# Performance work log

Measured on AMD Instinct MI355X. Metric: run time of the kernel, lower is better.

Reference implementation:

```python
import jax, jax.numpy as jnp
import numpy as np

B, N = 4096, 2048


def _nrmse(o, t):
    # o, t: [B, 1, N]. Per-sample RMSE over all non-batch elements,
    # normalized by per-sample (max - min) of the target.
    rmse = jnp.sqrt(jnp.mean((o - t) ** 2, axis=(1, 2)))        # [B]
    rng = jnp.max(t, axis=(1, 2)) - jnp.min(t, axis=(1, 2))     # [B]
    return rmse / rng


def setup_inputs() -> dict:
    key = jax.random.key(0)
    ks = jax.random.split(key, 6)
    names = ["o1", "t1", "o2", "t2", "o3", "t3"]
    return {n: jax.random.normal(k, (B, 1, N), dtype=jnp.float32) for n, k in zip(names, ks)}


def reference(o1, t1, o2, t2, o3, t3):
    loss = (0.5 * _nrmse(o1, t1)
            + 0.25 * _nrmse(o2, t2)
            + 0.25 * _nrmse(o3, t3))  # [B]
    return jnp.mean(loss)
```

## Files before the change

### kernel.cpp

```cpp
#include <hip/hip_runtime.h>
#include <math.h>

constexpr int N_ELEM = 2048;
constexpr int BATCH  = 4096;
constexpr int BLOCK  = 256;
constexpr int GRID1  = 1536;
constexpr int WAVES1 = GRID1 * (BLOCK / 64);
constexpr int TASKS  = 3 * BATCH;

__global__ __launch_bounds__(BLOCK)
void wnrmse_stage1(const float* __restrict__ o1, const float* __restrict__ t1,
                   const float* __restrict__ o2, const float* __restrict__ t2,
                   const float* __restrict__ o3, const float* __restrict__ t3,
                   float* __restrict__ partial)
{
    const int tid  = threadIdx.x;
    const int wave = tid >> 6;
    const int lane = tid & 63;
    const int gw   = blockIdx.x * (BLOCK / 64) + wave;

    const float* const os[3] = { o1, o2, o3 };
    const float* const ts[3] = { t1, t2, t3 };
    const float wgt[3] = { 0.50f, 0.25f, 0.25f };

    float local = 0.0f;

    for (int task = gw; task < TASKS; task += WAVES1) {
        const int pair = task >> 12;
        const int row  = task & (BATCH - 1);

        const float4* o4 = (const float4*)(os[pair] + (size_t)row * N_ELEM);
        const float4* t4 = (const float4*)(ts[pair] + (size_t)row * N_ELEM);

        float ssd  = 0.0f;
        float tmax = -INFINITY;
        float tmin =  INFINITY;

#pragma unroll
        for (int j = 0; j < (N_ELEM / 4) / 64; ++j) {
            const int i = lane + j * 64;
            float4 ov = o4[i];
            float4 tv = t4[i];
            float d0 = ov.x - tv.x;
            float d1 = ov.y - tv.y;
            float d2 = ov.z - tv.z;
            float d3 = ov.w - tv.w;
            ssd += d0 * d0 + d1 * d1 + d2 * d2 + d3 * d3;
            tmax = fmaxf(tmax, fmaxf(fmaxf(tv.x, tv.y), fmaxf(tv.z, tv.w)));
            tmin = fminf(tmin, fminf(fminf(tv.x, tv.y), fminf(tv.z, tv.w)));
        }

#pragma unroll
        for (int off = 32; off > 0; off >>= 1) {
            ssd  += __shfl_xor(ssd, off, 64);
            tmax  = fmaxf(tmax, __shfl_xor(tmax, off, 64));
            tmin  = fminf(tmin, __shfl_xor(tmin, off, 64));
        }

        float rmse = sqrtf(ssd * (1.0f / (float)N_ELEM));
        local += wgt[pair] * rmse / (tmax - tmin);
    }

    __shared__ float s_part[BLOCK / 64];
    if (lane == 0) s_part[wave] = local;
    __syncthreads();
    if (tid == 0) {
        partial[blockIdx.x] = s_part[0] + s_part[1] + s_part[2] + s_part[3];
    }
}

__global__ __launch_bounds__(BLOCK)
void wnrmse_stage2(const float* __restrict__ partial, float* __restrict__ out)
{
    const int tid = threadIdx.x;
    float s = 0.0f;
    for (int i = tid; i < GRID1; i += BLOCK) s += partial[i];

#pragma unroll
    for (int off = 32; off > 0; off >>= 1) s += __shfl_xor(s, off, 64);

    __shared__ float s_part[BLOCK / 64];
    const int wave = tid >> 6;
    const int lane = tid & 63;
    if (lane == 0) s_part[wave] = s;
    __syncthreads();
    if (tid == 0) {
        float tot = s_part[0] + s_part[1] + s_part[2] + s_part[3];
        out[0] = tot * (1.0f / (float)BATCH);
    }
}

extern "C" void kernel_launch(void* const* d_in, const int* in_sizes, int n_in,
                              void* d_out, int out_size, void* d_ws, size_t ws_size,
                              hipStream_t stream) {
    const float* o1 = (const float*)d_in[0];
    const float* t1 = (const float*)d_in[1];
    const float* o2 = (const float*)d_in[2];
    const float* t2 = (const float*)d_in[3];
    const float* o3 = (const float*)d_in[4];
    const float* t3 = (const float*)d_in[5];
    float* out     = (float*)d_out;
    float* partial = (float*)d_ws;

    wnrmse_stage1<<<GRID1, BLOCK, 0, stream>>>(o1, t1, o2, t2, o3, t3, partial);
    wnrmse_stage2<<<1, BLOCK, 0, stream>>>(partial, out);
}
```

Before: 203.3 us.

## Launch one wave per row and batch all row loads before reducing

Replaces the grid-stride loop over rows with one wave per row, growing the grid to 3072 blocks. All 16 float4 loads for a row are issued up front into registers, and the squared-difference sum is split across four accumulators. The aim is more memory-level parallelism and shorter dependency chains in a bandwidth-bound reduction. In exchange it raises register use and the stage-2 partial count, and adds block launch and scheduling overhead.

```diff
diff --git a/kernel.cpp b/kernel.cpp
--- a/kernel.cpp
+++ b/kernel.cpp
@@ -4,9 +4,8 @@
 constexpr int N_ELEM = 2048;
 constexpr int BATCH  = 4096;
 constexpr int BLOCK  = 256;
-constexpr int GRID1  = 1536;
-constexpr int WAVES1 = GRID1 * (BLOCK / 64);
 constexpr int TASKS  = 3 * BATCH;
+constexpr int GRID1  = TASKS / (BLOCK / 64);
 
 __global__ __launch_bounds__(BLOCK)
 void wnrmse_stage1(const float* __restrict__ o1, const float* __restrict__ t1,
@@ -17,52 +16,56 @@
     const int tid  = threadIdx.x;
     const int wave = tid >> 6;
     const int lane = tid & 63;
-    const int gw   = blockIdx.x * (BLOCK / 64) + wave;
+    const int task = blockIdx.x * (BLOCK / 64) + wave;
 
-    const float* const os[3] = { o1, o2, o3 };
-    const float* const ts[3] = { t1, t2, t3 };
-    const float wgt[3] = { 0.50f, 0.25f, 0.25f };
+    const int pair = task >> 12;
+    const int row  = task & (BATCH - 1);
 
-    float local = 0.0f;
+    const float* o;
+    const float* t;
+    float w;
+    if (pair == 0)      { o = o1; t = t1; w = 0.50f; }
+    else if (pair == 1) { o = o2; t = t2; w = 0.25f; }
+    else                { o = o3; t = t3; w = 0.25f; }
 
-    for (int task = gw; task < TASKS; task += WAVES1) {
-        const int pair = task >> 12;
-        const int row  = task & (BATCH - 1);
+    const float4* o4 = (const float4*)(o + (size_t)row * N_ELEM);
+    const float4* t4 = (const float4*)(t + (size_t)row * N_ELEM);
 
-        const float4* o4 = (const float4*)(os[pair] + (size_t)row * N_ELEM);
-        const float4* t4 = (const float4*)(ts[pair] + (size_t)row * N_ELEM);
+    float4 ov[8], tv[8];
+#pragma unroll
+    for (int j = 0; j < 8; ++j) ov[j] = o4[lane + j * 64];
+#pragma unroll
+    for (int j = 0; j < 8; ++j) tv[j] = t4[lane + j * 64];
 
-        float ssd  = 0.0f;
-        float tmax = -INFINITY;
-        float tmin =  INFINITY;
+    float s0 = 0.f, s1 = 0.f, s2 = 0.f, s3 = 0.f;
+    float tmax = -INFINITY, tmin = INFINITY;
+#pragma unroll
+    for (int j = 0; j < 8; ++j) {
+        float d0 = ov[j].x - tv[j].x;
+        float d1 = ov[j].y - tv[j].y;
+        float d2 = ov[j].z - tv[j].z;
+        float d3 = ov[j].w - tv[j].w;
+        s0 += d0 * d0;
+        s1 += d1 * d1;
+        s2 += d2 * d2;
+        s3 += d3 * d3;
+        tmax = fmaxf(tmax, fmaxf(fmaxf(tv[j].x, tv[j].y), fmaxf(tv[j].z, tv[j].w)));
+        tmin = fminf(tmin, fminf(fminf(tv[j].x, tv[j].y), fminf(tv[j].z, tv[j].w)));
+    }
+    float ssd = (s0 + s1) + (s2 + s3);
 
 #pragma unroll
-        for (int j = 0; j < (N_ELEM / 4) / 64; ++j) {
-            const int i = lane + j * 64;
-            float4 ov = o4[i];
-            float4 tv = t4[i];
-            float d0 = ov.x - tv.x;
-            float d1 = ov.y - tv.y;
-            float d2 = ov.z - tv.z;
-            float d3 = ov.w - tv.w;
-            ssd += d0 * d0 + d1 * d1 + d2 * d2 + d3 * d3;
-            tmax = fmaxf(tmax, fmaxf(fmaxf(tv.x, tv.y), fmaxf(tv.z, tv.w)));
-            tmin = fminf(tmin, fminf(fminf(tv.x, tv.y), fminf(tv.z, tv.w)));
-        }
-
-#pragma unroll
-        for (int off = 32; off > 0; off >>= 1) {
-            ssd  += __shfl_xor(ssd, off, 64);
-            tmax  = fmaxf(tmax, __shfl_xor(tmax, off, 64));
-            tmin  = fminf(tmin, __shfl_xor(tmin, off, 64));
-        }
-
-        float rmse = sqrtf(ssd * (1.0f / (float)N_ELEM));
-        local += wgt[pair] * rmse / (tmax - tmin);
+    for (int off = 32; off > 0; off >>= 1) {
+        ssd  += __shfl_xor(ssd, off, 64);
+        tmax  = fmaxf(tmax, __shfl_xor(tmax, off, 64));
+        tmin  = fminf(tmin, __shfl_xor(tmin, off, 64));
     }
 
     __shared__ float s_part[BLOCK / 64];
-    if (lane == 0) s_part[wave] = local;
+    if (lane == 0) {
+        float rmse = sqrtf(ssd * (1.0f / (float)N_ELEM));
+        s_part[wave] = w * rmse / (tmax - tmin);
+    }
     __syncthreads();
     if (tid == 0) {
         partial[blockIdx.x] = s_part[0] + s_part[1] + s_part[2] + s_part[3];
```

Result: no change. 205.7 us (+1.2%).
